# Kernel tuning notes

Hardware: AMD Instinct MI355X
Metric: run time of the kernel (lower is better)

The kernel has to match this reference:

```python
import jax, jax.numpy as jnp
import numpy as np

N_AGENTS = 50000  # number of batch elements (agents); fixed num_segments
N_NEIGHBORS = 1600000  # total ragged neighbors flattened (avg degree 32)
STATE_DIM = 64
PHI_HID = 64
PHI_OUT = 64
RHO_HID = 64
ACT_DIM = 2


def setup_inputs() -> dict:
    key = jax.random.key(0)
    ks = jax.random.split(key, 6)
    s = lambda fan_in: 1.0 / np.sqrt(fan_in)
    neighbors = jax.random.normal(ks[0], (N_NEIGHBORS, STATE_DIM), dtype=jnp.float32)
    phi_w1 = jax.random.normal(ks[1], (STATE_DIM, PHI_HID), dtype=jnp.float32) * s(STATE_DIM)
    phi_b1 = jnp.zeros((PHI_HID,), dtype=jnp.float32)
    phi_w2 = jax.random.normal(ks[2], (PHI_HID, PHI_OUT), dtype=jnp.float32) * s(PHI_HID)
    phi_b2 = jnp.zeros((PHI_OUT,), dtype=jnp.float32)
    rho_w1 = jax.random.normal(ks[3], (PHI_OUT, RHO_HID), dtype=jnp.float32) * s(PHI_OUT)
    rho_b1 = jnp.zeros((RHO_HID,), dtype=jnp.float32)
    rho_w2 = jax.random.normal(ks[4], (RHO_HID, ACT_DIM), dtype=jnp.float32) * s(RHO_HID)
    rho_b2 = jnp.zeros((ACT_DIM,), dtype=jnp.float32)
    segment_ids = jnp.sort(jax.random.randint(ks[5], (N_NEIGHBORS,), 0, N_AGENTS, dtype=jnp.int32))
    return {
        "neighbors": neighbors,
        "phi_w1": phi_w1, "phi_b1": phi_b1, "phi_w2": phi_w2, "phi_b2": phi_b2,
        "rho_w1": rho_w1, "rho_b1": rho_b1, "rho_w2": rho_w2, "rho_b2": rho_b2,
        "segment_ids": segment_ids,
    }


def reference(neighbors, phi_w1, phi_b1, phi_w2, phi_b2,
              rho_w1, rho_b1, rho_w2, rho_b2, segment_ids):
    # phi MLP applied to every neighbor feature (vectorized over the flat ragged axis)
    h = jax.nn.relu(neighbors @ phi_w1 + phi_b1)          # [N_NEIGHBORS, PHI_HID]
    h = h @ phi_w2 + phi_b2                               # [N_NEIGHBORS, PHI_OUT]
    # per-agent sum over variable-length neighbor sets (the Python double loop in torch)
    summ = jax.ops.segment_sum(h, segment_ids, num_segments=N_AGENTS)  # [N_AGENTS, PHI_OUT]
    # rho MLP on pooled features
    r = jax.nn.relu(summ @ rho_w1 + rho_b1)               # [N_AGENTS, RHO_HID]
    return r @ rho_w2 + rho_b2                            # [N_AGENTS, ACT_DIM]
```

## Files before the change

kernel.cpp:

```cpp
#include <hip/hip_runtime.h>
#include <hip/hip_bf16.h>

#define N_AGENTS 50000
#define N_NEI    1600000
#define ROWS     128
#define PHI_TILES (N_NEI / ROWS)
#define PHI_GRID  1024

typedef __bf16 bf16_t;
typedef __attribute__((ext_vector_type(8))) __bf16 bf16x8;
typedef __attribute__((ext_vector_type(4))) float  f32x4;

#define SA 72
#define SO 66

__global__ __launch_bounds__(256, 3) void phi_kernel(
    const float* __restrict__ nb,
    const float* __restrict__ w1g, const float* __restrict__ b1g,
    const float* __restrict__ w2g, const float* __restrict__ b2g,
    const int* __restrict__ seg, float* __restrict__ summ)
{
  __shared__ __align__(16) union {
    struct {
      bf16_t A[ROWS * SA];
      bf16_t Wt[2][64 * SA];
    } s;
    float outb[ROWS * SO];
  } u;
  __shared__ int sid[ROWS + 4];

  const int tid  = threadIdx.x;
  const int w    = tid >> 6;
  const int lane = tid & 63;
  const int m16  = lane & 15;
  const int q    = lane >> 4;
  const int rb   = w * 32;

  for (int i = tid; i < 4096; i += 256) {
    int k = i >> 6, n = i & 63;
    u.s.Wt[0][n * SA + k] = (bf16_t)w1g[i];
    u.s.Wt[1][n * SA + k] = (bf16_t)w2g[i];
  }
  float b1r[4], b2r[4];
  #pragma unroll
  for (int tn = 0; tn < 4; ++tn) {
    b1r[tn] = b1g[tn * 16 + m16];
    b2r[tn] = b2g[tn * 16 + m16];
  }
  __syncthreads();

  bf16x8 bf1[4][2], bf2[4][2];
  #pragma unroll
  for (int tn = 0; tn < 4; ++tn)
    #pragma unroll
    for (int kb = 0; kb < 2; ++kb) {
      bf1[tn][kb] = *(const bf16x8*)&u.s.Wt[0][(tn * 16 + m16) * SA + kb * 32 + q * 8];
      bf2[tn][kb] = *(const bf16x8*)&u.s.Wt[1][(tn * 16 + m16) * SA + kb * 32 + q * 8];
    }

  for (int t = blockIdx.x; t < PHI_TILES; t += gridDim.x) {
    const int base_row = t * ROWS;

    if (tid < ROWS) sid[tid] = seg[base_row + tid];
    {
      const float4* np4 = (const float4*)(nb + (size_t)base_row * 64);
      #pragma unroll
      for (int it = 0; it < 4; ++it) {
        int j = tid * 2 + it * 512;
        float4 v0 = np4[j], v1 = np4[j + 1];
        int row = j >> 4, col = (j & 15) * 4;
        bf16x8 p = { (bf16_t)v0.x, (bf16_t)v0.y, (bf16_t)v0.z, (bf16_t)v0.w,
                     (bf16_t)v1.x, (bf16_t)v1.y, (bf16_t)v1.z, (bf16_t)v1.w };
        *(bf16x8*)&u.s.A[row * SA + col] = p;
      }
    }
    __syncthreads();

    bf16x8 afr[2][2];
    f32x4  acc[2][4];
    #pragma unroll
    for (int tm = 0; tm < 2; ++tm)
      #pragma unroll
      for (int kb = 0; kb < 2; ++kb)
        afr[tm][kb] = *(const bf16x8*)&u.s.A[(rb + tm * 16 + m16) * SA + kb * 32 + q * 8];
    #pragma unroll
    for (int tm = 0; tm < 2; ++tm)
      #pragma unroll
      for (int tn = 0; tn < 4; ++tn) {
        f32x4 a = {0.f, 0.f, 0.f, 0.f};
        a = __builtin_amdgcn_mfma_f32_16x16x32_bf16(afr[tm][0], bf1[tn][0], a, 0, 0, 0);
        a = __builtin_amdgcn_mfma_f32_16x16x32_bf16(afr[tm][1], bf1[tn][1], a, 0, 0, 0);
        acc[tm][tn] = a;
      }
    #pragma unroll
    for (int tm = 0; tm < 2; ++tm)
      #pragma unroll
      for (int tn = 0; tn < 4; ++tn) {
        float bv = b1r[tn];
        #pragma unroll
        for (int i = 0; i < 4; ++i) {
          float hv = fmaxf(acc[tm][tn][i] + bv, 0.f);
          u.s.A[(rb + tm * 16 + q * 4 + i) * SA + tn * 16 + m16] = (bf16_t)hv;
        }
      }

    #pragma unroll
    for (int tm = 0; tm < 2; ++tm)
      #pragma unroll
      for (int kb = 0; kb < 2; ++kb)
        afr[tm][kb] = *(const bf16x8*)&u.s.A[(rb + tm * 16 + m16) * SA + kb * 32 + q * 8];
    __syncthreads();

    #pragma unroll
    for (int tm = 0; tm < 2; ++tm)
      #pragma unroll
      for (int tn = 0; tn < 4; ++tn) {
        f32x4 a = {0.f, 0.f, 0.f, 0.f};
        a = __builtin_amdgcn_mfma_f32_16x16x32_bf16(afr[tm][0], bf2[tn][0], a, 0, 0, 0);
        a = __builtin_amdgcn_mfma_f32_16x16x32_bf16(afr[tm][1], bf2[tn][1], a, 0, 0, 0);
        acc[tm][tn] = a;
      }
    #pragma unroll
    for (int tm = 0; tm < 2; ++tm)
      #pragma unroll
      for (int tn = 0; tn < 4; ++tn) {
        float bv = b2r[tn];
        #pragma unroll
        for (int i = 0; i < 4; ++i)
          u.outb[(rb + tm * 16 + q * 4 + i) * SO + tn * 16 + m16] = acc[tm][tn][i] + bv;
      }

    float racc = 0.f;
    for (int r = rb; r < rb + 32; ++r) {
      racc += u.outb[r * SO + lane];
      int sr = sid[r];
      if (r == rb + 31 || sid[r + 1] != sr) {
        atomicAdd(summ + (size_t)sr * 64 + lane, racc);
        racc = 0.f;
      }
    }
    __syncthreads();
  }
}

__global__ __launch_bounds__(256) void rho_kernel(
    const float* __restrict__ summ,
    const float* __restrict__ w1g, const float* __restrict__ b1g,
    const float* __restrict__ w2g, const float* __restrict__ b2g,
    float* __restrict__ out)
{
  __shared__ float sw1t[64 * 68];
  __shared__ float sw2[128];
  __shared__ float sb1[64];
  __shared__ float sb2[2];
  const int tid = threadIdx.x;
  for (int i = tid; i < 4096; i += 256) {
    int n = i >> 6, k = i & 63;
    sw1t[n * 68 + k] = w1g[k * 64 + n];
  }
  if (tid < 128) sw2[tid] = w2g[tid];
  if (tid < 64)  sb1[tid] = b1g[tid];
  if (tid < 2)   sb2[tid] = b2g[tid];
  __syncthreads();

  int a = blockIdx.x * 256 + tid;
  if (a >= N_AGENTS) return;

  float x[64];
  const float4* xr = (const float4*)(summ + (size_t)a * 64);
  #pragma unroll
  for (int i = 0; i < 16; ++i) {
    float4 v = xr[i];
    x[4*i] = v.x; x[4*i+1] = v.y; x[4*i+2] = v.z; x[4*i+3] = v.w;
  }

  float o0 = sb2[0], o1 = sb2[1];
  for (int n = 0; n < 64; ++n) {
    const float4* wr = (const float4*)&sw1t[n * 68];
    float a0 = sb1[n], a1 = 0.f, a2 = 0.f, a3 = 0.f;
    #pragma unroll
    for (int kq = 0; kq < 16; ++kq) {
      float4 wv = wr[kq];
      a0 = fmaf(x[4*kq],     wv.x, a0);
      a1 = fmaf(x[4*kq + 1], wv.y, a1);
      a2 = fmaf(x[4*kq + 2], wv.z, a2);
      a3 = fmaf(x[4*kq + 3], wv.w, a3);
    }
    float h = fmaxf((a0 + a1) + (a2 + a3), 0.f);
    o0 = fmaf(h, sw2[2 * n],     o0);
    o1 = fmaf(h, sw2[2 * n + 1], o1);
  }
  *(float2*)(out + (size_t)a * 2) = make_float2(o0, o1);
}

extern "C" void kernel_launch(void* const* d_in, const int* in_sizes, int n_in,
                              void* d_out, int out_size, void* d_ws, size_t ws_size,
                              hipStream_t stream) {
  const float* neighbors = (const float*)d_in[0];
  const float* phi_w1    = (const float*)d_in[1];
  const float* phi_b1    = (const float*)d_in[2];
  const float* phi_w2    = (const float*)d_in[3];
  const float* phi_b2    = (const float*)d_in[4];
  const float* rho_w1    = (const float*)d_in[5];
  const float* rho_b1    = (const float*)d_in[6];
  const float* rho_w2    = (const float*)d_in[7];
  const float* rho_b2    = (const float*)d_in[8];
  const int*   seg       = (const int*)d_in[9];
  float* out  = (float*)d_out;
  float* summ = (float*)d_ws;

  hipMemsetAsync(summ, 0, (size_t)N_AGENTS * 64 * sizeof(float), stream);
  phi_kernel<<<PHI_GRID, 256, 0, stream>>>(neighbors, phi_w1, phi_b1,
                                           phi_w2, phi_b2, seg, summ);
  rho_kernel<<<(N_AGENTS + 255) / 256, 256, 0, stream>>>(summ, rho_w1, rho_b1,
                                                         rho_w2, rho_b2, out);
}
```

Baseline: 628.1 us.

## Replace persistent phi loop with one block per tile and pre-transposed bf16 weights

Drops the persistent grid-stride loop in favour of one block per 128-row tile, so more blocks can overlap loads with compute. A small prep kernel converts and transposes the phi weights to bf16 in workspace, so each block copies them with vector loads instead of doing strided conversion. The MFMA operands are swapped so each lane's accumulator holds contiguous columns, which allows vectorised bias-add and LDS stores. The cost is that every block reloads the weights and biases, plus an extra kernel launch.

Measured after the change: 601.4 us. -4.2%, faster.

```diff
diff --git a/kernel.cpp b/kernel.cpp
--- a/kernel.cpp
+++ b/kernel.cpp
@@ -4,20 +4,40 @@
 #define N_AGENTS 50000
 #define N_NEI    1600000
 #define ROWS     128
-#define PHI_TILES (N_NEI / ROWS)
-#define PHI_GRID  1024
+#define PHI_BLOCKS (N_NEI / ROWS)
 
 typedef __bf16 bf16_t;
 typedef __attribute__((ext_vector_type(8))) __bf16 bf16x8;
+typedef __attribute__((ext_vector_type(4))) __bf16 bf16x4;
+typedef __attribute__((ext_vector_type(2))) __bf16 bf16x2;
 typedef __attribute__((ext_vector_type(4))) float  f32x4;
 
 #define SA 72
-#define SO 66
-
-__global__ __launch_bounds__(256, 3) void phi_kernel(
+#define SO 68
+
+#define SUMM_BYTES ((size_t)N_AGENTS * 64 * sizeof(float))
+
+__global__ __launch_bounds__(256) void prep_weights(
+    const float* __restrict__ w1g, const float* __restrict__ w2g,
+    bf16_t* __restrict__ gWt)
+{
+  __shared__ float s[4096];
+  const int tid = threadIdx.x;
+  const float* src = blockIdx.x ? w2g : w1g;
+  bf16_t* dst = gWt + blockIdx.x * 4096;
+  for (int i = tid; i < 4096; i += 256) s[i] = src[i];
+  __syncthreads();
+  for (int i = tid; i < 2048; i += 256) {
+    int n = i >> 5, k2 = (i & 31) * 2;
+    bf16x2 p = { (bf16_t)s[k2 * 64 + n], (bf16_t)s[(k2 + 1) * 64 + n] };
+    *(bf16x2*)&dst[n * 64 + k2] = p;
+  }
+}
+
+__global__ __launch_bounds__(256) void phi_kernel(
     const float* __restrict__ nb,
-    const float* __restrict__ w1g, const float* __restrict__ b1g,
-    const float* __restrict__ w2g, const float* __restrict__ b2g,
+    const bf16_t* __restrict__ gWt,
+    const float* __restrict__ b1g, const float* __restrict__ b2g,
     const int* __restrict__ seg, float* __restrict__ summ)
 {
   __shared__ __align__(16) union {
@@ -35,111 +55,111 @@
   const int m16  = lane & 15;
   const int q    = lane >> 4;
   const int rb   = w * 32;
-
-  for (int i = tid; i < 4096; i += 256) {
-    int k = i >> 6, n = i & 63;
-    u.s.Wt[0][n * SA + k] = (bf16_t)w1g[i];
-    u.s.Wt[1][n * SA + k] = (bf16_t)w2g[i];
-  }
-  float b1r[4], b2r[4];
-  #pragma unroll
-  for (int tn = 0; tn < 4; ++tn) {
-    b1r[tn] = b1g[tn * 16 + m16];
-    b2r[tn] = b2g[tn * 16 + m16];
-  }
-  __syncthreads();
-
-  bf16x8 bf1[4][2], bf2[4][2];
-  #pragma unroll
-  for (int tn = 0; tn < 4; ++tn)
-    #pragma unroll
-    for (int kb = 0; kb < 2; ++kb) {
-      bf1[tn][kb] = *(const bf16x8*)&u.s.Wt[0][(tn * 16 + m16) * SA + kb * 32 + q * 8];
-      bf2[tn][kb] = *(const bf16x8*)&u.s.Wt[1][(tn * 16 + m16) * SA + kb * 32 + q * 8];
-    }
-
-  for (int t = blockIdx.x; t < PHI_TILES; t += gridDim.x) {
-    const int base_row = t * ROWS;
-
-    if (tid < ROWS) sid[tid] = seg[base_row + tid];
-    {
-      const float4* np4 = (const float4*)(nb + (size_t)base_row * 64);
-      #pragma unroll
-      for (int it = 0; it < 4; ++it) {
-        int j = tid * 2 + it * 512;
-        float4 v0 = np4[j], v1 = np4[j + 1];
-        int row = j >> 4, col = (j & 15) * 4;
-        bf16x8 p = { (bf16_t)v0.x, (bf16_t)v0.y, (bf16_t)v0.z, (bf16_t)v0.w,
-                     (bf16_t)v1.x, (bf16_t)v1.y, (bf16_t)v1.z, (bf16_t)v1.w };
-        *(bf16x8*)&u.s.A[row * SA + col] = p;
-      }
-    }
-    __syncthreads();
-
-    bf16x8 afr[2][2];
-    f32x4  acc[2][4];
-    #pragma unroll
-    for (int tm = 0; tm < 2; ++tm)
-      #pragma unroll
-      for (int kb = 0; kb < 2; ++kb)
-        afr[tm][kb] = *(const bf16x8*)&u.s.A[(rb + tm * 16 + m16) * SA + kb * 32 + q * 8];
-    #pragma unroll
-    for (int tm = 0; tm < 2; ++tm)
-      #pragma unroll
-      for (int tn = 0; tn < 4; ++tn) {
-        f32x4 a = {0.f, 0.f, 0.f, 0.f};
-        a = __builtin_amdgcn_mfma_f32_16x16x32_bf16(afr[tm][0], bf1[tn][0], a, 0, 0, 0);
-        a = __builtin_amdgcn_mfma_f32_16x16x32_bf16(afr[tm][1], bf1[tn][1], a, 0, 0, 0);
-        acc[tm][tn] = a;
-      }
-    #pragma unroll
-    for (int tm = 0; tm < 2; ++tm)
-      #pragma unroll
-      for (int tn = 0; tn < 4; ++tn) {
-        float bv = b1r[tn];
-        #pragma unroll
-        for (int i = 0; i < 4; ++i) {
-          float hv = fmaxf(acc[tm][tn][i] + bv, 0.f);
-          u.s.A[(rb + tm * 16 + q * 4 + i) * SA + tn * 16 + m16] = (bf16_t)hv;
-        }
-      }
-
-    #pragma unroll
-    for (int tm = 0; tm < 2; ++tm)
-      #pragma unroll
-      for (int kb = 0; kb < 2; ++kb)
-        afr[tm][kb] = *(const bf16x8*)&u.s.A[(rb + tm * 16 + m16) * SA + kb * 32 + q * 8];
-    __syncthreads();
-
-    #pragma unroll
-    for (int tm = 0; tm < 2; ++tm)
-      #pragma unroll
-      for (int tn = 0; tn < 4; ++tn) {
-        f32x4 a = {0.f, 0.f, 0.f, 0.f};
-        a = __builtin_amdgcn_mfma_f32_16x16x32_bf16(afr[tm][0], bf2[tn][0], a, 0, 0, 0);
-        a = __builtin_amdgcn_mfma_f32_16x16x32_bf16(afr[tm][1], bf2[tn][1], a, 0, 0, 0);
-        acc[tm][tn] = a;
-      }
-    #pragma unroll
-    for (int tm = 0; tm < 2; ++tm)
-      #pragma unroll
-      for (int tn = 0; tn < 4; ++tn) {
-        float bv = b2r[tn];
-        #pragma unroll
-        for (int i = 0; i < 4; ++i)
-          u.outb[(rb + tm * 16 + q * 4 + i) * SO + tn * 16 + m16] = acc[tm][tn][i] + bv;
-      }
-
-    float racc = 0.f;
-    for (int r = rb; r < rb + 32; ++r) {
-      racc += u.outb[r * SO + lane];
-      int sr = sid[r];
-      if (r == rb + 31 || sid[r + 1] != sr) {
-        atomicAdd(summ + (size_t)sr * 64 + lane, racc);
-        racc = 0.f;
-      }
-    }
-    __syncthreads();
+  const int base_row = blockIdx.x * ROWS;
+
+  if (tid < ROWS) sid[tid] = seg[base_row + tid];
+
+  for (int i = tid; i < 1024; i += 256) {
+    int mat = i >> 9, r = i & 511;
+    int n = r >> 3, c = r & 7;
+    bf16x8 v = *(const bf16x8*)&gWt[mat * 4096 + n * 64 + c * 8];
+    *(bf16x8*)&u.s.Wt[mat][n * SA + c * 8] = v;
+  }
+
+  float4 b1v[4];
+  #pragma unroll
+  for (int tn = 0; tn < 4; ++tn)
+    b1v[tn] = *(const float4*)(b1g + tn * 16 + q * 4);
+
+  {
+    const float4* np4 = (const float4*)(nb + (size_t)base_row * 64);
+    #pragma unroll
+    for (int it = 0; it < 4; ++it) {
+      int j = tid * 2 + it * 512;
+      float4 v0 = np4[j], v1 = np4[j + 1];
+      int row = j >> 4, col = (j & 15) * 4;
+      bf16x8 p = { (bf16_t)v0.x, (bf16_t)v0.y, (bf16_t)v0.z, (bf16_t)v0.w,
+                   (bf16_t)v1.x, (bf16_t)v1.y, (bf16_t)v1.z, (bf16_t)v1.w };
+      *(bf16x8*)&u.s.A[row * SA + col] = p;
+    }
+  }
+  __syncthreads();
+
+  bf16x8 wfr[4][2], xfr[2][2];
+  f32x4  acc[2][4];
+
+  #pragma unroll
+  for (int tn = 0; tn < 4; ++tn)
+    #pragma unroll
+    for (int kb = 0; kb < 2; ++kb)
+      wfr[tn][kb] = *(const bf16x8*)&u.s.Wt[0][(tn * 16 + m16) * SA + kb * 32 + q * 8];
+  #pragma unroll
+  for (int tm = 0; tm < 2; ++tm)
+    #pragma unroll
+    for (int kb = 0; kb < 2; ++kb)
+      xfr[tm][kb] = *(const bf16x8*)&u.s.A[(rb + tm * 16 + m16) * SA + kb * 32 + q * 8];
+  #pragma unroll
+  for (int tm = 0; tm < 2; ++tm)
+    #pragma unroll
+    for (int tn = 0; tn < 4; ++tn) {
+      f32x4 a = {0.f, 0.f, 0.f, 0.f};
+      a = __builtin_amdgcn_mfma_f32_16x16x32_bf16(wfr[tn][0], xfr[tm][0], a, 0, 0, 0);
+      a = __builtin_amdgcn_mfma_f32_16x16x32_bf16(wfr[tn][1], xfr[tm][1], a, 0, 0, 0);
+      acc[tm][tn] = a;
+    }
+  #pragma unroll
+  for (int tm = 0; tm < 2; ++tm)
+    #pragma unroll
+    for (int tn = 0; tn < 4; ++tn) {
+      bf16x4 p = { (bf16_t)fmaxf(acc[tm][tn][0] + b1v[tn].x, 0.f),
+                   (bf16_t)fmaxf(acc[tm][tn][1] + b1v[tn].y, 0.f),
+                   (bf16_t)fmaxf(acc[tm][tn][2] + b1v[tn].z, 0.f),
+                   (bf16_t)fmaxf(acc[tm][tn][3] + b1v[tn].w, 0.f) };
+      *(bf16x4*)&u.s.A[(rb + tm * 16 + m16) * SA + tn * 16 + q * 4] = p;
+    }
+
+  float4 b2v[4];
+  #pragma unroll
+  for (int tn = 0; tn < 4; ++tn)
+    b2v[tn] = *(const float4*)(b2g + tn * 16 + q * 4);
+  #pragma unroll
+  for (int tn = 0; tn < 4; ++tn)
+    #pragma unroll
+    for (int kb = 0; kb < 2; ++kb)
+      wfr[tn][kb] = *(const bf16x8*)&u.s.Wt[1][(tn * 16 + m16) * SA + kb * 32 + q * 8];
+  #pragma unroll
+  for (int tm = 0; tm < 2; ++tm)
+    #pragma unroll
+    for (int kb = 0; kb < 2; ++kb)
+      xfr[tm][kb] = *(const bf16x8*)&u.s.A[(rb + tm * 16 + m16) * SA + kb * 32 + q * 8];
+  __syncthreads();
+
+  #pragma unroll
+  for (int tm = 0; tm < 2; ++tm)
+    #pragma unroll
+    for (int tn = 0; tn < 4; ++tn) {
+      f32x4 a = {0.f, 0.f, 0.f, 0.f};
+      a = __builtin_amdgcn_mfma_f32_16x16x32_bf16(wfr[tn][0], xfr[tm][0], a, 0, 0, 0);
+      a = __builtin_amdgcn_mfma_f32_16x16x32_bf16(wfr[tn][1], xfr[tm][1], a, 0, 0, 0);
+      acc[tm][tn] = a;
+    }
+  #pragma unroll
+  for (int tm = 0; tm < 2; ++tm)
+    #pragma unroll
+    for (int tn = 0; tn < 4; ++tn) {
+      f32x4 o = { acc[tm][tn][0] + b2v[tn].x, acc[tm][tn][1] + b2v[tn].y,
+                  acc[tm][tn][2] + b2v[tn].z, acc[tm][tn][3] + b2v[tn].w };
+      *(f32x4*)&u.outb[(rb + tm * 16 + m16) * SO + tn * 16 + q * 4] = o;
+    }
+
+  float racc = 0.f;
+  for (int r = rb; r < rb + 32; ++r) {
+    racc += u.outb[r * SO + lane];
+    int sr = sid[r];
+    if (r == rb + 31 || sid[r + 1] != sr) {
+      atomicAdd(summ + (size_t)sr * 64 + lane, racc);
+      racc = 0.f;
+    }
   }
 }
 
@@ -208,10 +228,12 @@
   const int*   seg       = (const int*)d_in[9];
   float* out  = (float*)d_out;
   float* summ = (float*)d_ws;
-
-  hipMemsetAsync(summ, 0, (size_t)N_AGENTS * 64 * sizeof(float), stream);
-  phi_kernel<<<PHI_GRID, 256, 0, stream>>>(neighbors, phi_w1, phi_b1,
-                                           phi_w2, phi_b2, seg, summ);
+  bf16_t* gWt = (bf16_t*)((char*)d_ws + SUMM_BYTES);
+
+  hipMemsetAsync(summ, 0, SUMM_BYTES, stream);
+  prep_weights<<<2, 256, 0, stream>>>(phi_w1, phi_w2, gWt);
+  phi_kernel<<<PHI_BLOCKS, 256, 0, stream>>>(neighbors, gWt, phi_b1, phi_b2,
+                                             seg, summ);
   rho_kernel<<<(N_AGENTS + 255) / 256, 256, 0, stream>>>(summ, rho_w1, rho_b1,
                                                          rho_w2, rho_b2, out);
 }
```
